# Performance work log

Hardware: AMD Instinct MI355X
Metric: run time of the kernel (lower is better)

Reference implementation:

```python
import jax, jax.numpy as jnp
import numpy as np

DIM = 512; HEADS = 8; DH = 64; M = 256; ITERS = 6; LN_EPS = 1e-5; RES_K = 33


def layernorm(x, g, b):
    mu = jnp.mean(x, -1, keepdims=True)
    var = jnp.mean((x - mu) ** 2, -1, keepdims=True)
    return (x - mu) * jax.lax.rsqrt(var + LN_EPS) * g + b


def moore_penrose_pinv(a, iters=ITERS):
    # Newton-Schulz iteration, matching nystrom_attention.moore_penrose_iter_pinv
    ab = jnp.abs(a)
    z = jnp.swapaxes(a, -1, -2) / (jnp.max(jnp.sum(ab, -1)) * jnp.max(jnp.sum(ab, -2)))
    I = jnp.eye(a.shape[-1], dtype=a.dtype)
    for _ in range(iters):
        az = a @ z
        z = 0.25 * z @ (13. * I - az @ (15. * I - az @ (7. * I - az)))
    return z


def dwconv2d(x, w, b, k):
    # x: [B,C,H,W], w: [C,1,k,k] depthwise
    C = x.shape[1]
    y = jax.lax.conv_general_dilated(x, w, (1, 1), [(k // 2, k // 2), (k // 2, k // 2)],
                                     feature_group_count=C,
                                     dimension_numbers=('NCHW', 'OIHW', 'NCHW'))
    return y + b[None, :, None, None]


def nystrom_attention(x, qkv_w, out_w, out_b, res_w):
    b, n, d = x.shape
    pad = (M - n % M) % M
    xp = jnp.pad(x, ((0, 0), (pad, 0), (0, 0)))  # pad at front, as in reference impl
    npd = n + pad
    qkv = xp @ qkv_w  # [b, npd, 3d]
    q, k, v = jnp.split(qkv, 3, axis=-1)
    to_heads = lambda t: t.reshape(b, npd, HEADS, DH).transpose(0, 2, 1, 3)  # bhnd
    q = to_heads(q) * (DH ** -0.5)
    k = to_heads(k)
    v = to_heads(v)
    l = npd // M  # tokens per landmark
    q_l = q.reshape(b, HEADS, M, l, DH).mean(3)  # [b,h,M,dh]
    k_l = k.reshape(b, HEADS, M, l, DH).mean(3)
    a1 = jax.nn.softmax(jnp.einsum('bhid,bhjd->bhij', q, k_l), axis=-1)    # [b,h,n,M]
    a2 = jax.nn.softmax(jnp.einsum('bhid,bhjd->bhij', q_l, k_l), axis=-1)  # [b,h,M,M]
    a3 = jax.nn.softmax(jnp.einsum('bhid,bhjd->bhij', q_l, k), axis=-1)    # [b,h,M,n]
    out = (a1 @ moore_penrose_pinv(a2)) @ (a3 @ v)  # [b,h,n,dh]
    # residual depthwise conv over sequence dim of v (channels = heads)
    res = jax.lax.conv_general_dilated(v, res_w, (1, 1), [(RES_K // 2, RES_K // 2), (0, 0)],
                                       feature_group_count=HEADS,
                                       dimension_numbers=('NCHW', 'OIHW', 'NCHW'))
    out = out + res
    out = out.transpose(0, 2, 1, 3).reshape(b, npd, d) @ out_w + out_b
    return out[:, -n:]


def _forward(x, fc1_w, fc1_b, cls_token,
             l1_norm_g, l1_norm_b, l1_qkv_w, l1_out_w, l1_out_b, l1_res_w,
             ppeg_w7, ppeg_b7, ppeg_w5, ppeg_b5, ppeg_w3, ppeg_b3,
             l2_norm_g, l2_norm_b, l2_qkv_w, l2_out_w, l2_out_b, l2_res_w,
             norm_g, norm_b, fc2_w, fc2_b):
    h = jax.nn.relu(x @ fc1_w + fc1_b)  # [B,N,C]
    B, N, C = h.shape
    Hs = int(np.ceil(np.sqrt(N)))
    add = Hs * Hs - N
    h = jnp.concatenate([h, h[:, :add]], axis=1)  # square padding
    cls = jnp.broadcast_to(cls_token, (B, 1, C))
    h = jnp.concatenate([cls, h], axis=1)  # [B, Hs*Hs+1, C]
    # TransLayer 1
    h = h + nystrom_attention(layernorm(h, l1_norm_g, l1_norm_b), l1_qkv_w, l1_out_w, l1_out_b, l1_res_w)
    # PPEG
    cls_t, feat = h[:, 0], h[:, 1:]
    cf = feat.transpose(0, 2, 1).reshape(B, C, Hs, Hs)
    y = cf + dwconv2d(cf, ppeg_w7, ppeg_b7, 7) + dwconv2d(cf, ppeg_w5, ppeg_b5, 5) + dwconv2d(cf, ppeg_w3, ppeg_b3, 3)
    h = jnp.concatenate([cls_t[:, None], y.reshape(B, C, Hs * Hs).transpose(0, 2, 1)], axis=1)
    # TransLayer 2
    h = h + nystrom_attention(layernorm(h, l2_norm_g, l2_norm_b), l2_qkv_w, l2_out_w, l2_out_b, l2_res_w)
    h = layernorm(h, norm_g, norm_b)[:, 0]
    return h @ fc2_w + fc2_b  # logits [B, n_classes]


def setup_inputs() -> dict:
    key = jax.random.key(0)
    ks = jax.random.split(key, 32)
    B, N, IN, C, NC = 1, 16384, 1024, 512, 4
    s = 0.02
    f32 = jnp.float32
    d = {}
    d['x'] = jax.random.normal(ks[0], (B, N, IN), f32)
    d['fc1_w'] = jax.random.normal(ks[1], (IN, C), f32) * s
    d['fc1_b'] = jnp.zeros((C,), f32)
    d['cls_token'] = jax.random.normal(ks[2], (1, 1, C), f32)
    for i, p in enumerate(['l1', 'l2']):
        kk = jax.random.split(ks[3 + i], 8)
        d[p + '_norm_g'] = jnp.ones((C,), f32)
        d[p + '_norm_b'] = jnp.zeros((C,), f32)
        d[p + '_qkv_w'] = jax.random.normal(kk[0], (C, 3 * C), f32) * s
        d[p + '_out_w'] = jax.random.normal(kk[1], (C, C), f32) * s
        d[p + '_out_b'] = jnp.zeros((C,), f32)
        d[p + '_res_w'] = jax.random.normal(kk[2], (HEADS, 1, RES_K, 1), f32) * s
    for i, k_sz in enumerate([7, 5, 3]):
        d[f'ppeg_w{k_sz}'] = jax.random.normal(ks[8 + i], (C, 1, k_sz, k_sz), f32) * s
        d[f'ppeg_b{k_sz}'] = jnp.zeros((C,), f32)
    d['norm_g'] = jnp.ones((C,), f32)
    d['norm_b'] = jnp.zeros((C,), f32)
    d['fc2_w'] = jax.random.normal(ks[12], (C, NC), f32) * s
    d['fc2_b'] = jnp.zeros((NC,), f32)
    return d


def reference(x, fc1_w, fc1_b, cls_token,
              l1_norm_g, l1_norm_b, l1_qkv_w, l1_out_w, l1_out_b, l1_res_w,
              ppeg_w7, ppeg_b7, ppeg_w5, ppeg_b5, ppeg_w3, ppeg_b3,
              l2_norm_g, l2_norm_b, l2_qkv_w, l2_out_w, l2_out_b, l2_res_w,
              norm_g, norm_b, fc2_w, fc2_b):
    return _forward(x, fc1_w, fc1_b, cls_token,
                    l1_norm_g, l1_norm_b, l1_qkv_w, l1_out_w, l1_out_b, l1_res_w,
                    ppeg_w7, ppeg_b7, ppeg_w5, ppeg_b5, ppeg_w3, ppeg_b3,
                    l2_norm_g, l2_norm_b, l2_qkv_w, l2_out_w, l2_out_b, l2_res_w,
                    norm_g, norm_b, fc2_w, fc2_b)
```

## Files before the change

### kernel.cpp

```cpp
#include <hip/hip_runtime.h>


#define NT 16385
#define NP 16640
#define PAD 255
#define CDIM 512
#define HEADS 8
#define DH 64
#define LM 256
#define LSEG 65

typedef unsigned short u16;
typedef unsigned int u32;
typedef __attribute__((ext_vector_type(8))) short bf16x8;
typedef __attribute__((ext_vector_type(4))) float f32x4;

__device__ __forceinline__ u16 f2b(float f){
  u32 u = __float_as_uint(f);
  u32 r = (u + 0x7FFFu + ((u >> 16) & 1u)) >> 16;
  return (u16)r;
}
__device__ __forceinline__ float b2f(u16 h){ return __uint_as_float(((u32)h) << 16); }

__device__ __forceinline__ void gload16(const u16* g, u16* l){
  __builtin_amdgcn_global_load_lds(
      (const __attribute__((address_space(1))) u32*)g,
      (__attribute__((address_space(3))) u32*)l, 16, 0, 0);
}

__device__ __forceinline__ int xcd_swz(int orig, int nwg){
  int qn = nwg >> 3, rn = nwg & 7;
  int xcd = orig & 7, sid = orig >> 3;
  return (xcd < rn ? xcd * (qn + 1) : rn * (qn + 1) + (xcd - rn) * qn) + sid;
}

__device__ __forceinline__ float wredSum(float v){
#pragma unroll
  for (int o = 32; o > 0; o >>= 1) v += __shfl_xor(v, o, 64);
  return v;
}
__device__ __forceinline__ float wredMax(float v){
#pragma unroll
  for (int o = 32; o > 0; o >>= 1) v = fmaxf(v, __shfl_xor(v, o, 64));
  return v;
}
__device__ __forceinline__ float bredSum(float v, float* sm){
  v = wredSum(v);
  int w = threadIdx.x >> 6, l = threadIdx.x & 63;
  __syncthreads();
  if (l == 0) sm[w] = v;
  __syncthreads();
  return sm[0] + sm[1] + sm[2] + sm[3];
}
__device__ __forceinline__ float bredMax(float v, float* sm){
  v = wredMax(v);
  int w = threadIdx.x >> 6, l = threadIdx.x & 63;
  __syncthreads();
  if (l == 0) sm[w] = v;
  __syncthreads();
  return fmaxf(fmaxf(sm[0], sm[1]), fmaxf(sm[2], sm[3]));
}

__global__ __launch_bounds__(256) void copy_cls_k(const float* __restrict__ cls,
                                                  float* __restrict__ h){
  h[threadIdx.x] = cls[threadIdx.x];
  h[threadIdx.x + 256] = cls[threadIdx.x + 256];
}
__global__ __launch_bounds__(256) void cvtbf_k(const float* __restrict__ in,
                                               u16* __restrict__ out, long long n){
  long long i = ((long long)blockIdx.x * 256 + threadIdx.x) * 4;
  long long stride = (long long)gridDim.x * 256 * 4;
  for (; i < n; i += stride){
    float4 v = *(const float4*)(in + i);
    out[i]     = f2b(v.x);
    out[i + 1] = f2b(v.y);
    out[i + 2] = f2b(v.z);
    out[i + 3] = f2b(v.w);
  }
}
__global__ __launch_bounds__(256) void tcbf_k(const float* __restrict__ in,
    u16* __restrict__ out, int R, int C, int ldin, int ldout,
    long long sIn, long long sOut){
  __shared__ float t[32][33];
  in += (long long)blockIdx.z * sIn; out += (long long)blockIdx.z * sOut;
  int c0 = blockIdx.x * 32, r0 = blockIdx.y * 32;
  int x = threadIdx.x & 31, y = threadIdx.x >> 5;
  for (int yy = y; yy < 32; yy += 8){
    int r = r0 + yy, c = c0 + x;
    if (r < R && c < C) t[yy][x] = in[(long long)r * ldin + c];
  }
  __syncthreads();
  for (int yy = y; yy < 32; yy += 8){
    int c = c0 + yy, r = r0 + x;
    if (c < C && r < R) out[(long long)c * ldout + r] = f2b(t[x][yy]);
  }
}

#define GB_STOREBF 1
#define GB_RELU    2
#define GB_ACCUM   4
#define GB_ATOMIC  8
#define GB_QSCALE  16
#define GB_SWZ     32

template<int DBUF>
__global__ __launch_bounds__(256) void gemmbf_k(
    const u16* __restrict__ A, const u16* __restrict__ B, void* __restrict__ Cv,
    int M, int N, int K, int lda, int ldb, int ldc,
    long long sA, long long sB, long long sC,
    const float* __restrict__ bias, const float* __restrict__ rowdiv, int sRow,
    float alpha, int flags, int ksplit, u16* __restrict__ vt)
{
  __shared__ __align__(16) u16 sh[DBUF ? 32768 : 16384];
  int zb = blockIdx.z / ksplit;
  int ks = blockIdx.z - zb * ksplit;
  A += (long long)zb * sA; B += (long long)zb * sB;
  float* Cf = (float*)Cv + (long long)zb * sC;
  u16*   Ch = (u16*)Cv + (long long)zb * sC;
  int klen = K / ksplit;
  int kbeg = ks * klen, kend = kbeg + klen;
  int tid = threadIdx.x;
  int w = tid >> 6, l = tid & 63;
  int row0, col0;
  if (flags & GB_SWZ){
    int gx = gridDim.x;
    int swz = xcd_swz(blockIdx.y * gx + blockIdx.x, gx * gridDim.y);
    row0 = (swz / gx) * 128; col0 = (swz % gx) * 128;
  } else {
    row0 = blockIdx.y * 128; col0 = blockIdx.x * 128;
  }
  int r8 = l >> 3;
  int csrc = ((l & 7) ^ r8) * 8;
  f32x4 acc[2][8];
#pragma unroll
  for (int i = 0; i < 2; i++)
#pragma unroll
    for (int j = 0; j < 8; j++) acc[i][j] = (f32x4){0.f, 0.f, 0.f, 0.f};

  int mrow = l & 15, q8 = l >> 4;

  auto STAGE = [&](int buf, int k0){
    u16* Asb = sh + buf * 16384;
    u16* Bsb = Asb + 8192;
#pragma unroll
    for (int c = 0; c < 4; c++){
      int r = w * 32 + c * 8;
      int gm = row0 + r + r8; if (gm >= M) gm = M - 1;
      gload16(A + (long long)gm * lda + k0 + csrc, &Asb[r * 64]);
      int gn = col0 + r + r8; if (gn >= N) gn = N - 1;
      gload16(B + (long long)gn * ldb + k0 + csrc, &Bsb[r * 64]);
    }
  };
  auto COMPUTE = [&](int buf){
    const u16* Asb = sh + buf * 16384;
    const u16* Bsb = Asb + 8192;
#pragma unroll
    for (int ks2 = 0; ks2 < 2; ks2++){
      int kc = ks2 * 4 + q8;
      bf16x8 af[2], bfr[8];
#pragma unroll
      for (int i = 0; i < 2; i++){
        int r = w * 32 + i * 16 + mrow;
        af[i] = *(const bf16x8*)&Asb[r * 64 + ((kc ^ (r & 7)) * 8)];
      }
#pragma unroll
      for (int j = 0; j < 8; j++){
        int r = j * 16 + mrow;
        bfr[j] = *(const bf16x8*)&Bsb[r * 64 + ((kc ^ (r & 7)) * 8)];
      }
#pragma unroll
      for (int i = 0; i < 2; i++)
#pragma unroll
        for (int j = 0; j < 8; j++)
          acc[i][j] = __builtin_amdgcn_mfma_f32_16x16x32_bf16(af[i], bfr[j], acc[i][j], 0, 0, 0);
    }
  };

  if constexpr (DBUF){
    STAGE(0, kbeg);
    __syncthreads();
    int cur = 0;
    for (int k0 = kbeg; k0 < kend; k0 += 64){
      if (k0 + 64 < kend) STAGE(cur ^ 1, k0 + 64);
      COMPUTE(cur);
      __syncthreads();
      cur ^= 1;
    }
  } else {
    for (int k0 = kbeg; k0 < kend; k0 += 64){
      STAGE(0, k0);
      __syncthreads();
      COMPUTE(0);
      __syncthreads();
    }
  }

  if (flags & GB_STOREBF){
#pragma unroll
    for (int p = 0; p < 2; p++){
      __syncthreads();
#pragma unroll
      for (int i = 0; i < 2; i++)
#pragma unroll
        for (int r = 0; r < 4; r++){
          int lrow = w * 32 + i * 16 + q8 * 4 + r;
          int gm = row0 + lrow;
          float rd = rowdiv ? rowdiv[(long long)zb * sRow + gm] : 1.f;
#pragma unroll
          for (int jj = 0; jj < 4; jj++){
            int j = p * 4 + jj;
            int gn = col0 + j * 16 + mrow;
            float v = alpha * acc[i][j][r];
            if ((flags & GB_QSCALE) && gn < 512) v *= 0.125f;
            if (rowdiv) v /= rd;
            if (bias) v += bias[gn];
            if (flags & GB_RELU) v = fmaxf(v, 0.f);
            sh[lrow * 72 + (j * 16 + mrow - p * 64)] = f2b(v);
          }
        }
      __syncthreads();
#pragma unroll
      for (int it = 0; it < 4; it++){
        int cidx = tid + it * 256;
        int rr = cidx >> 3, c8 = (cidx & 7) * 8;
        int gm = row0 + rr;
        if (gm < M)
          *(uint4*)(Ch + (long long)gm * ldc + col0 + p * 64 + c8) =
              *(const uint4*)&sh[rr * 72 + c8];
      }
    }
    if (vt && col0 >= 1024){
      int gc0 = col0 - 1024;
#pragma unroll
      for (int p = 0; p < 2; p++){
        __syncthreads();
#pragma unroll
        for (int i = 0; i < 2; i++)
#pragma unroll
          for (int r = 0; r < 4; r++){
            int lrow = w * 32 + i * 16 + q8 * 4 + r;
#pragma unroll
            for (int jj = 0; jj < 4; jj++){
              int j = p * 4 + jj;
              int lcol = j * 16 + mrow - p * 64;
              sh[lcol * 136 + lrow] = f2b(alpha * acc[i][j][r]);
            }
          }
        __syncthreads();
#pragma unroll
        for (int it = 0; it < 4; it++){
          int cidx = tid + it * 256;
          int cc = cidx >> 4, rc = (cidx & 15) * 8;
          *(uint4*)(vt + (long long)(gc0 + p * 64 + cc) * NP + row0 + rc) =
              *(const uint4*)&sh[cc * 136 + rc];
        }
      }
    }
    return;
  }

  if constexpr (DBUF){
    if (!(flags & GB_ATOMIC)){
      float* shf = (float*)sh;
#pragma unroll
      for (int p = 0; p < 2; p++){
        __syncthreads();
#pragma unroll
        for (int i = 0; i < 2; i++)
#pragma unroll
          for (int r = 0; r < 4; r++){
            int lrow = w * 32 + i * 16 + q8 * 4 + r;
            int gm = row0 + lrow;
            int gmc = (gm < M) ? gm : M - 1;
            float rd = rowdiv ? rowdiv[(long long)zb * sRow + gmc] : 1.f;
#pragma unroll
            for (int jj = 0; jj < 4; jj++){
              int j = p * 4 + jj;
              int gn = col0 + j * 16 + mrow;
              float v = alpha * acc[i][j][r];
              if ((flags & GB_QSCALE) && gn < 512) v *= 0.125f;
              if (rowdiv) v /= rd;
              if (bias) v += bias[gn];
              if (flags & GB_RELU) v = fmaxf(v, 0.f);
              shf[lrow * 68 + (j * 16 + mrow - p * 64)] = v;
            }
          }
        __syncthreads();
#pragma unroll
        for (int it = 0; it < 8; it++){
          int cidx = tid + it * 256;
          int rr = cidx >> 4, c4 = (cidx & 15) * 4;
          int gm = row0 + rr;
          if (gm >= M) continue;
          int gn = col0 + p * 64 + c4;
          if (gn + 3 < N){
            float4* dst = (float4*)(Cf + (long long)gm * ldc + gn);
            float4 vv = *(const float4*)&shf[rr * 68 + c4];
            if (flags & GB_ACCUM){
              float4 o = *dst;
              vv.x += o.x; vv.y += o.y; vv.z += o.z; vv.w += o.w;
            }
            *dst = vv;
          } else {
            for (int e = 0; e < 4; e++){
              if (gn + e >= N) break;
              float v = shf[rr * 68 + c4 + e];
              if (flags & GB_ACCUM) Cf[(long long)gm * ldc + gn + e] += v;
              else Cf[(long long)gm * ldc + gn + e] = v;
            }
          }
        }
      }
      return;
    }
  }

#pragma unroll
  for (int i = 0; i < 2; i++){
#pragma unroll
    for (int r = 0; r < 4; r++){
      int gm = row0 + w * 32 + i * 16 + q8 * 4 + r;
      if (gm >= M) continue;
      float rd = rowdiv ? rowdiv[(long long)zb * sRow + gm] : 1.f;
#pragma unroll
      for (int j = 0; j < 8; j++){
        int gn = col0 + j * 16 + mrow;
        if (gn >= N) continue;
        float v = alpha * acc[i][j][r];
        if ((flags & GB_QSCALE) && gn < 512) v *= 0.125f;
        if (rowdiv) v /= rd;
        if (bias) v += bias[gn];
        if (flags & GB_RELU) v = fmaxf(v, 0.f);
        long long ci = (long long)gm * ldc + gn;
        if (flags & GB_ATOMIC) atomicAdd(&Cf[ci], v);
        else if (flags & GB_ACCUM) Cf[ci] += v;
        else Cf[ci] = v;
      }
    }
  }
}

__device__ __forceinline__ void pinv_core(
    u16* lds, int cb, int rb, int head,
    const u16* __restrict__ Ah, const u16* __restrict__ Al,
    const u16* __restrict__ BTh, const u16* __restrict__ BTl,
    u16* __restrict__ Chh, u16* __restrict__ Cll,
    u16* __restrict__ CTh, u16* __restrict__ CTl,
    float* __restrict__ Cf,
    const u16* __restrict__ Avh, const u16* __restrict__ Avl,
    float dterm, float sterm, float eterm)
{
  u16* Ash = lds;
  u16* Asl = lds + 4096;
  u16* Bsh = lds + 8192;
  u16* Bsl = lds + 16384;
  long long off = (long long)head << 16;
  int tid = threadIdx.x, w = tid >> 6, l = tid & 63;
  int row0 = rb * 64, col0 = cb * 128;
  int r8 = l >> 3;
  int csrc = ((l & 7) ^ r8) * 8;
  int mrow = l & 15, q8 = l >> 4;
  f32x4 acc[8];
#pragma unroll
  for (int j = 0; j < 8; j++) acc[j] = (f32x4){0.f, 0.f, 0.f, 0.f};

  for (int k0 = 0; k0 < 256; k0 += 64){
#pragma unroll
    for (int c = 0; c < 2; c++){
      int r = w * 16 + c * 8;
      long long ga = off + (long long)(row0 + r + r8) * 256 + k0 + csrc;
      gload16(Ah + ga, &Ash[r * 64]);
      gload16(Al + ga, &Asl[r * 64]);
    }
#pragma unroll
    for (int c = 0; c < 4; c++){
      int r = w * 32 + c * 8;
      long long gb = off + (long long)(col0 + r + r8) * 256 + k0 + csrc;
      gload16(BTh + gb, &Bsh[r * 64]);
      gload16(BTl + gb, &Bsl[r * 64]);
    }
    __syncthreads();
#pragma unroll
    for (int ks2 = 0; ks2 < 2; ks2++){
      int kc = ks2 * 4 + q8;
      bf16x8 ah, al, bh[8], bl[8];
      {
        int r = w * 16 + mrow;
        int idx = r * 64 + ((kc ^ (r & 7)) * 8);
        ah = *(const bf16x8*)&Ash[idx];
        al = *(const bf16x8*)&Asl[idx];
      }
#pragma unroll
      for (int j = 0; j < 8; j++){
        int r = j * 16 + mrow;
        int idx = r * 64 + ((kc ^ (r & 7)) * 8);
        bh[j] = *(const bf16x8*)&Bsh[idx];
        bl[j] = *(const bf16x8*)&Bsl[idx];
      }
#pragma unroll
      for (int j = 0; j < 8; j++){
        acc[j] = __builtin_amdgcn_mfma_f32_16x16x32_bf16(ah, bh[j], acc[j], 0, 0, 0);
        acc[j] = __builtin_amdgcn_mfma_f32_16x16x32_bf16(ah, bl[j], acc[j], 0, 0, 0);
        acc[j] = __builtin_amdgcn_mfma_f32_16x16x32_bf16(al, bh[j], acc[j], 0, 0, 0);
      }
    }
    __syncthreads();
  }
#pragma unroll
  for (int r = 0; r < 4; r++){
    int gm = row0 + w * 16 + q8 * 4 + r;
#pragma unroll
    for (int j = 0; j < 8; j++){
      int gn = col0 + j * 16 + mrow;
      float v = sterm * acc[j][r];
      if (Avh){
        long long ai = off + (long long)gm * 256 + gn;
        v += eterm * (b2f(Avh[ai]) + b2f(Avl[ai]));
      }
      if (gm == gn) v += dterm;
      acc[j][r] = v;
      long long ci = off + (long long)gm * 256 + gn;
      if (Cf) Cf[ci] = v;
      if (Chh){
        u16 hi = f2b(v);
        Chh[ci] = hi;
        Cll[ci] = f2b(v - b2f(hi));
      }
    }
  }
  if (CTh){
#pragma unroll
    for (int pass = 0; pass < 2; pass++){
      __syncthreads();
#pragma unroll
      for (int r = 0; r < 4; r++){
        int lm = w * 16 + q8 * 4 + r;
#pragma unroll
        for (int j = 0; j < 8; j++){
          int ln = j * 16 + mrow;
          float v = acc[j][r];
          u16 hi = f2b(v);
          lds[ln * 72 + lm] = (pass == 0) ? hi : f2b(v - b2f(hi));
        }
      }
      __syncthreads();
      u16* dst = (pass == 0) ? CTh : CTl;
#pragma unroll
      for (int it = 0; it < 4; it++){
        int cidx = tid + it * 256;
        int rr = cidx >> 3;
        int cc = (cidx & 7) * 8;
        *(uint4*)(dst + off + (long long)(col0 + rr) * 256 + row0 + cc) =
            *(const uint4*)&lds[rr * 72 + cc];
      }
    }
  }
}

__global__ __launch_bounds__(256) void pinvh_k(
    const u16* __restrict__ Ah, const u16* __restrict__ Al,
    const u16* __restrict__ BTh, const u16* __restrict__ BTl,
    u16* __restrict__ Chh, u16* __restrict__ Cll,
    u16* __restrict__ CTh, u16* __restrict__ CTl,
    float* __restrict__ Cf,
    const u16* __restrict__ Avh, const u16* __restrict__ Avl,
    float dterm, float sterm, float eterm)
{
  __shared__ __align__(16) u16 lds[24576];
  pinv_core(lds, blockIdx.x, blockIdx.y, blockIdx.z,
            Ah, Al, BTh, BTl, Chh, Cll, CTh, CTl, Cf, Avh, Avl,
            dterm, sterm, eterm);
}
__global__ __launch_bounds__(256) void pinv2_k(
    const u16* __restrict__ azh, const u16* __restrict__ azl,
    const u16* __restrict__ azTh, const u16* __restrict__ azTl,
    const u16* __restrict__ zh, const u16* __restrict__ zl,
    u16* __restrict__ tATh, u16* __restrict__ tATl,
    u16* __restrict__ zah, u16* __restrict__ zal)
{
  __shared__ __align__(16) u16 lds[24576];
  int head = blockIdx.z & 7;
  if (blockIdx.z < 8)
    pinv_core(lds, blockIdx.x, blockIdx.y, head, azh, azl, azTh, azTl,
              nullptr, nullptr, tATh, tATl, nullptr, azh, azl, 15.f, 1.f, -7.f);
  else
    pinv_core(lds, blockIdx.x, blockIdx.y, head, zh, zl, azTh, azTl,
              zah, zal, nullptr, nullptr, nullptr, nullptr, nullptr, 0.f, 1.f, 0.f);
}

#define GF_TRANSB 1
__global__ __launch_bounds__(256) void gemm_k(
    const float* __restrict__ A, const float* __restrict__ B, float* __restrict__ C,
    int M, int N, int K, int lda, int ldb, int ldc,
    long long sA, long long sB, long long sC, float alpha, int flags)
{
  __shared__ __align__(16) float As[16][68];
  __shared__ __align__(16) float Bs[16][68];
  int zb = blockIdx.z;
  A += (long long)zb * sA; B += (long long)zb * sB; C += (long long)zb * sC;
  int tid = threadIdx.x;
  int tx = tid & 15, ty = tid >> 4;
  int row0 = blockIdx.y * 64, col0 = blockIdx.x * 64;
  float acc[4][4] = {};
  for (int k0 = 0; k0 < K; k0 += 16){
#pragma unroll
    for (int i = 0; i < 4; i++){
      int idx = tid + i * 256;
      int mm = idx >> 4, kk = idx & 15;
      int gm = row0 + mm;
      As[kk][mm] = (gm < M) ? A[(long long)gm * lda + (k0 + kk)] : 0.f;
    }
    if (!(flags & GF_TRANSB)){
#pragma unroll
      for (int i = 0; i < 4; i++){
        int idx = tid + i * 256;
        int kk = idx >> 6, nn = idx & 63;
        int gn = col0 + nn;
        Bs[kk][nn] = (gn < N) ? B[(long long)(k0 + kk) * ldb + gn] : 0.f;
      }
    } else {
#pragma unroll
      for (int i = 0; i < 4; i++){
        int idx = tid + i * 256;
        int nn = idx >> 4, kk = idx & 15;
        int gn = col0 + nn;
        Bs[kk][nn] = (gn < N) ? B[(long long)gn * ldb + (k0 + kk)] : 0.f;
      }
    }
    __syncthreads();
#pragma unroll
    for (int kk = 0; kk < 16; kk++){
      float4 av = *(const float4*)&As[kk][ty * 4];
      float4 bv = *(const float4*)&Bs[kk][tx * 4];
      float a[4] = {av.x, av.y, av.z, av.w};
      float b[4] = {bv.x, bv.y, bv.z, bv.w};
#pragma unroll
      for (int i = 0; i < 4; i++)
#pragma unroll
        for (int j = 0; j < 4; j++)
          acc[i][j] = fmaf(a[i], b[j], acc[i][j]);
    }
    __syncthreads();
  }
#pragma unroll
  for (int i = 0; i < 4; i++){
    int gm = row0 + ty * 4 + i;
    if (gm >= M) continue;
#pragma unroll
    for (int j = 0; j < 4; j++){
      int gn = col0 + tx * 4 + j;
      if (gn >= N) continue;
      C[(long long)gm * ldc + gn] = alpha * acc[i][j];
    }
  }
}

__global__ __launch_bounds__(256) void fattn_k(
    const u16* __restrict__ Qp, int ldq,
    const u16* __restrict__ Kp, int ldk,
    const u16* __restrict__ Vp, int ldv,
    long long sQh, long long sKh, long long sVh,
    int keysPerChunk,
    u16* __restrict__ outB, int ldo,
    float* __restrict__ O3, float* __restrict__ ML3, int nchunks, int qrows,
    int mode)
{
  __shared__ u16 Qs[64][72];
  __shared__ u16 Ks[128][72];
  __shared__ u16 Vs[64][136];
  __shared__ u16 Ps[4][16][136];
  int tid = threadIdx.x;
  int w = tid >> 6, l = tid & 63;
  int mrow = l & 15, q8 = l >> 4;
  int gx = gridDim.x, gy = gridDim.y;
  int swz = xcd_swz((blockIdx.z * gy + blockIdx.y) * gx + blockIdx.x,
                    gx * gy * gridDim.z);
  int qt = swz % gx, t2 = swz / gx;
  int ch = t2 % gy, h = t2 / gy;
  const u16* Q = Qp + (long long)h * sQh;
  const u16* K = Kp + (long long)h * sKh;
  const u16* V = Vp + (long long)h * sVh;
  int q0 = qt * 64;
  for (int i = tid; i < 512; i += 256){
    int r = i >> 3, c = (i & 7) * 8;
    *(uint4*)&Qs[r][c] = *(const uint4*)(Q + (long long)(q0 + r) * ldq + c);
  }
  float m_st[4], l_st[4];
  f32x4 acc_o[4];
#pragma unroll
  for (int r = 0; r < 4; r++){
    m_st[r] = -3.0e38f; l_st[r] = 0.f;
    acc_o[r] = (f32x4){0.f, 0.f, 0.f, 0.f};
  }
  int kbase = ch * keysPerChunk;
  for (int kt = 0; kt < keysPerChunk; kt += 128){
    for (int i = tid; i < 1024; i += 256){
      int r = i >> 3, c = (i & 7) * 8;
      *(uint4*)&Ks[r][c] = *(const uint4*)(K + (long long)(kbase + kt + r) * ldk + c);
    }
    for (int i = tid; i < 1024; i += 256){
      int r = i >> 4, c = (i & 15) * 8;
      *(uint4*)&Vs[r][c] = *(const uint4*)(V + (long long)r * ldv + kbase + kt + c);
    }
    __syncthreads();
    f32x4 accs[8];
#pragma unroll
    for (int j = 0; j < 8; j++) accs[j] = (f32x4){0.f, 0.f, 0.f, 0.f};
#pragma unroll
    for (int ks2 = 0; ks2 < 2; ks2++){
      bf16x8 af = *(const bf16x8*)&Qs[w * 16 + mrow][ks2 * 32 + q8 * 8];
#pragma unroll
      for (int j = 0; j < 8; j++){
        bf16x8 bfv = *(const bf16x8*)&Ks[j * 16 + mrow][ks2 * 32 + q8 * 8];
        accs[j] = __builtin_amdgcn_mfma_f32_16x16x32_bf16(af, bfv, accs[j], 0, 0, 0);
      }
    }
#pragma unroll
    for (int r = 0; r < 4; r++){
      float tm = -3.0e38f;
#pragma unroll
      for (int j = 0; j < 8; j++) tm = fmaxf(tm, accs[j][r]);
      tm = fmaxf(tm, __shfl_xor(tm, 1, 64));
      tm = fmaxf(tm, __shfl_xor(tm, 2, 64));
      tm = fmaxf(tm, __shfl_xor(tm, 4, 64));
      tm = fmaxf(tm, __shfl_xor(tm, 8, 64));
      float mn = fmaxf(m_st[r], tm);
      float al = __expf(m_st[r] - mn);
      m_st[r] = mn;
      float rs = 0.f;
#pragma unroll
      for (int j = 0; j < 8; j++){
        float e = __expf(accs[j][r] - mn);
        accs[j][r] = e;
        rs += e;
      }
      rs += __shfl_xor(rs, 1, 64);
      rs += __shfl_xor(rs, 2, 64);
      rs += __shfl_xor(rs, 4, 64);
      rs += __shfl_xor(rs, 8, 64);
      l_st[r] = al * l_st[r] + rs;
#pragma unroll
      for (int j = 0; j < 4; j++) acc_o[j][r] *= al;
    }
#pragma unroll
    for (int j = 0; j < 8; j++)
#pragma unroll
      for (int r = 0; r < 4; r++)
        Ps[w][q8 * 4 + r][j * 16 + mrow] = f2b(accs[j][r]);
    __syncthreads();
#pragma unroll
    for (int kc = 0; kc < 4; kc++){
      bf16x8 af = *(const bf16x8*)&Ps[w][mrow][kc * 32 + q8 * 8];
#pragma unroll
      for (int j = 0; j < 4; j++){
        bf16x8 bfv = *(const bf16x8*)&Vs[j * 16 + mrow][kc * 32 + q8 * 8];
        acc_o[j] = __builtin_amdgcn_mfma_f32_16x16x32_bf16(af, bfv, acc_o[j], 0, 0, 0);
      }
    }
    __syncthreads();
  }
  if (mode == 0){
#pragma unroll
    for (int r = 0; r < 4; r++){
      int grow = q0 + w * 16 + q8 * 4 + r;
      float inv = 1.f / l_st[r];
#pragma unroll
      for (int j = 0; j < 4; j++)
        outB[(long long)grow * ldo + h * 64 + j * 16 + mrow] = f2b(acc_o[j][r] * inv);
    }
  } else {
#pragma unroll
    for (int r = 0; r < 4; r++){
      int row = q0 + w * 16 + q8 * 4 + r;
      long long b = ((long long)h * nchunks + ch) * qrows + row;
#pragma unroll
      for (int j = 0; j < 4; j++)
        O3[b * 64 + j * 16 + mrow] = acc_o[j][r];
      if (mrow == 0){
        ML3[b * 2] = m_st[r];
        ML3[b * 2 + 1] = l_st[r];
      }
    }
  }
}

__global__ __launch_bounds__(256) void comb3_k(
    const float* __restrict__ O3, const float* __restrict__ ML3,
    float* __restrict__ a3v)
{
  int h = blockIdx.y;
  int row = blockIdx.x * 4 + (threadIdx.x >> 6);
  int d = threadIdx.x & 63;
  float m = -3.0e38f;
  for (int c = 0; c < 13; c++)
    m = fmaxf(m, ML3[(((long long)h * 13 + c) * 256 + row) * 2]);
  float l = 0.f, o = 0.f;
  for (int c = 0; c < 13; c++){
    long long b = ((long long)h * 13 + c) * 256 + row;
    float wgt = __expf(ML3[b * 2] - m);
    l += wgt * ML3[b * 2 + 1];
    o += wgt * O3[b * 64 + d];
  }
  a3v[((long long)h * 256 + row) * 64 + d] = o / l;
}

__global__ __launch_bounds__(256) void ln_pad_k(
    const float* __restrict__ h, const float* __restrict__ g,
    const float* __restrict__ b, u16* __restrict__ out)
{
  __shared__ float sm[4];
  int row = blockIdx.x, tid = threadIdx.x;
  u16* o = out + (long long)row * CDIM;
  if (row < PAD){ o[tid] = 0; o[tid + 256] = 0; return; }
  const float* x = h + (long long)(row - PAD) * CDIM;
  float v0 = x[tid], v1 = x[tid + 256];
  float s = bredSum(v0 + v1, sm);
  float s2 = bredSum(v0 * v0 + v1 * v1, sm);
  float mean = s * (1.f / 512.f);
  float var = s2 * (1.f / 512.f) - mean * mean;
  float rstd = rsqrtf(var + 1e-5f);
  o[tid] = f2b((v0 - mean) * rstd * g[tid] + b[tid]);
  o[tid + 256] = f2b((v1 - mean) * rstd * g[tid + 256] + b[tid + 256]);
}

__global__ __launch_bounds__(256) void landmark_k(
    const u16* __restrict__ qkv, float* __restrict__ ql, float* __restrict__ kl,
    u16* __restrict__ qlh, u16* __restrict__ klh)
{
  int m = blockIdx.x * 2 + (threadIdx.x >> 7);
  int c8 = (threadIdx.x & 127) * 8;
  const u16* base = qkv + (long long)(m * LSEG) * 1536 + c8;
  float s[8] = {};
  for (int j = 0; j < LSEG; j++){
    uint4 pk = *(const uint4*)(base + (long long)j * 1536);
    const u16* pv = (const u16*)&pk;
#pragma unroll
    for (int e = 0; e < 8; e++) s[e] += b2f(pv[e]);
  }
#pragma unroll
  for (int e = 0; e < 8; e++){
    int col = c8 + e;
    float v = s[e] * (1.f / 65.f);
    int h = (col & 511) >> 6, d = col & 63;
    int idx = (h * LM + m) * DH + d;
    if (col < 512){ ql[idx] = v; qlh[idx] = f2b(v); }
    else          { kl[idx] = v; klh[idx] = f2b(v); }
  }
}

__global__ __launch_bounds__(256) void softmax256_k(float* __restrict__ S,
    u16* __restrict__ a2h, u16* __restrict__ a2l, float* __restrict__ scal)
{
  __shared__ float sm[4];
  int i = blockIdx.x, h = blockIdx.y, j = threadIdx.x;
  if (i == 0 && h == 0 && j < 2) scal[j] = 0.f;
  long long idx = ((long long)h * LM + i) * 256 + j;
  float v = S[idx];
  float m = bredMax(v, sm);
  float e = __expf(v - m);
  float s = bredSum(e, sm);
  float p = e / s;
  S[idx] = p;
  u16 hi = f2b(p);
  a2h[idx] = hi;
  a2l[idx] = f2b(p - b2f(hi));
}

__global__ __launch_bounds__(256) void pinv_scal_k(
    const float* __restrict__ a2, float* __restrict__ scal)
{
  __shared__ float sm[4];
  int h = blockIdx.x, i = threadIdx.x;
  const float* Ah = a2 + (long long)h * 65536;
  float rs = 0.f, cs = 0.f;
  for (int j = 0; j < 256; j++){
    rs += fabsf(Ah[i * 256 + j]);
    cs += fabsf(Ah[j * 256 + i]);
  }
  float rmax = bredMax(rs, sm);
  __syncthreads();
  float cmax = bredMax(cs, sm);
  if (i == 0){
    atomicMax((int*)&scal[0], __float_as_int(rmax));
    atomicMax((int*)&scal[1], __float_as_int(cmax));
  }
}

__global__ __launch_bounds__(256) void z0_k(
    const float* __restrict__ a2, const float* __restrict__ scal,
    u16* __restrict__ zh, u16* __restrict__ zl,
    u16* __restrict__ zTh, u16* __restrict__ zTl)
{
  int ri = blockIdx.x, h = blockIdx.y, j = threadIdx.x;
  float inv = 1.f / (scal[0] * scal[1]);
  long long base = ((long long)h * LM + ri) * 256;
  float v = a2[base + j] * inv;
  u16 hi = f2b(v), lo = f2b(v - b2f(hi));
  zTh[base + j] = hi; zTl[base + j] = lo;
  long long tb = ((long long)h * LM + j) * 256 + ri;
  zh[tb] = hi; zl[tb] = lo;
}

__global__ __launch_bounds__(256) void resconv_k(
    const u16* __restrict__ vT, const float* __restrict__ rw,
    u16* __restrict__ attn)
{
  int c = blockIdx.x * 256 + threadIdx.x;
  int s0 = blockIdx.y * 8;
  int h = c >> 6;
  float w[33];
#pragma unroll
  for (int t = 0; t < 33; t++) w[t] = rw[h * 33 + t];
  float vr[40];
  const u16* vrow = vT + (long long)c * NP;
  if (s0 >= 16 && s0 + 24 <= NP){
#pragma unroll
    for (int q = 0; q < 5; q++){
      uint4 pk = *(const uint4*)(vrow + s0 - 16 + q * 8);
      const u16* pv = (const u16*)&pk;
#pragma unroll
      for (int e = 0; e < 8; e++) vr[q * 8 + e] = b2f(pv[e]);
    }
  } else {
#pragma unroll
    for (int j = 0; j < 40; j++){
      int s = s0 - 16 + j;
      vr[j] = (s >= 0 && s < NP) ? b2f(vrow[s]) : 0.f;
    }
  }
#pragma unroll
  for (int i = 0; i < 8; i++){
    float a = 0.f;
#pragma unroll
    for (int t = 0; t < 33; t++) a = fmaf(vr[i + t], w[t], a);
    long long idx = (long long)(s0 + i) * CDIM + c;
    attn[idx] = f2b(b2f(attn[idx]) + a);
  }
}

__global__ __launch_bounds__(256) void transpose_k(
    const float* __restrict__ in, float* __restrict__ out, int R, int Cc)
{
  __shared__ float t[32][33];
  int bx = blockIdx.x * 32, by = blockIdx.y * 32;
  int x = threadIdx.x & 31, y4 = threadIdx.x >> 5;
  for (int yy = y4; yy < 32; yy += 8){
    int r = by + yy, c = bx + x;
    if (r < R && c < Cc) t[yy][x] = in[(long long)r * Cc + c];
  }
  __syncthreads();
  for (int yy = y4; yy < 32; yy += 8){
    int r = bx + yy, c = by + x;
    if (r < Cc && c < R) out[(long long)r * R + c] = t[x][yy];
  }
}

__global__ __launch_bounds__(256) void ppeg_k(
    const float* __restrict__ cf, float* __restrict__ yt,
    const float* __restrict__ w7, const float* __restrict__ b7,
    const float* __restrict__ w5, const float* __restrict__ b5,
    const float* __restrict__ w3, const float* __restrict__ b3)
{
  __shared__ float tile[22][23];
  int c = blockIdx.z;
  int ty0 = blockIdx.y * 16, tx0 = blockIdx.x * 16;
  const float* img = cf + (long long)c * 16384;
  for (int i = threadIdx.x; i < 22 * 22; i += 256){
    int yy = i / 22, xx = i - yy * 22;
    int gy = ty0 - 3 + yy, gx = tx0 - 3 + xx;
    tile[yy][xx] = (gy >= 0 && gy < 128 && gx >= 0 && gx < 128) ? img[gy * 128 + gx] : 0.f;
  }
  __syncthreads();
  int lx = threadIdx.x & 15, ly = threadIdx.x >> 4;
  float o = tile[ly + 3][lx + 3] + b7[c] + b5[c] + b3[c];
  const float* W7 = w7 + c * 49;
#pragma unroll
  for (int ky = 0; ky < 7; ky++)
#pragma unroll
    for (int kx = 0; kx < 7; kx++)
      o = fmaf(tile[ly + ky][lx + kx], W7[ky * 7 + kx], o);
  const float* W5 = w5 + c * 25;
#pragma unroll
  for (int ky = 0; ky < 5; ky++)
#pragma unroll
    for (int kx = 0; kx < 5; kx++)
      o = fmaf(tile[ly + 1 + ky][lx + 1 + kx], W5[ky * 5 + kx], o);
  const float* W3 = w3 + c * 9;
#pragma unroll
  for (int ky = 0; ky < 3; ky++)
#pragma unroll
    for (int kx = 0; kx < 3; kx++)
      o = fmaf(tile[ly + 2 + ky][lx + 2 + kx], W3[ky * 3 + kx], o);
  yt[(long long)c * 16384 + (ty0 + ly) * 128 + (tx0 + lx)] = o;
}

__global__ __launch_bounds__(256) void final_k(
    const float* __restrict__ h, const float* __restrict__ g,
    const float* __restrict__ b, const float* __restrict__ w,
    const float* __restrict__ bias, float* __restrict__ out)
{
  __shared__ float sm[4];
  __shared__ float pj[256][4];
  int tid = threadIdx.x;
  float v0 = h[tid], v1 = h[tid + 256];
  float s = bredSum(v0 + v1, sm);
  float s2 = bredSum(v0 * v0 + v1 * v1, sm);
  float mean = s * (1.f / 512.f);
  float var = s2 * (1.f / 512.f) - mean * mean;
  float rstd = rsqrtf(var + 1e-5f);
  float n0 = (v0 - mean) * rstd * g[tid] + b[tid];
  float n1 = (v1 - mean) * rstd * g[tid + 256] + b[tid + 256];
#pragma unroll
  for (int j = 0; j < 4; j++)
    pj[tid][j] = n0 * w[tid * 4 + j] + n1 * w[(tid + 256) * 4 + j];
  __syncthreads();
  if (tid < 4){
    float acc = 0.f;
    for (int k = 0; k < 256; k++) acc += pj[k][tid];
    out[tid] = acc + bias[tid];
  }
}

static inline void gemmbf(hipStream_t st, const u16* A, const u16* B, void* C,
                          int M, int N, int K, int lda, int ldb, int ldc,
                          long long sA, long long sB, long long sC, int batch,
                          const float* bias, const float* rowdiv, int sRow,
                          float alpha, int flags, int ksplit, u16* vt, int dbuf)
{
  dim3 grid((N + 127) / 128, (M + 127) / 128, batch * ksplit);
  if (dbuf)
    gemmbf_k<1><<<grid, 256, 0, st>>>(A, B, C, M, N, K, lda, ldb, ldc, sA, sB, sC,
                                      bias, rowdiv, sRow, alpha, flags, ksplit, vt);
  else
    gemmbf_k<0><<<grid, 256, 0, st>>>(A, B, C, M, N, K, lda, ldb, ldc, sA, sB, sC,
                                      bias, rowdiv, sRow, alpha, flags, ksplit, vt);
}

#define B_H     0LL
#define B_XQ    33556480LL
#define B_ATTN  50595840LL
#define B_QKV   67635200LL
#define B_VT    118753280LL
#define B_O3    135792640LL
#define B_ML3   142608384LL
#define B_QL    169871360LL
#define B_KL    170395648LL
#define B_QLH   170919936LL
#define B_KLH   171182080LL
#define B_A2    171444224LL
#define B_PV2   173541376LL
#define B_A3V   184027136LL
#define B_Z2    184551424LL
#define B_Z2T   185075712LL
#define B_SCAL  185604096LL
#define B_W1T   185604352LL
#define B_WQT   186652928LL
#define B_WOT   188225792LL
#define WS_REQ  188750080LL
#define MB1     1048576LL

extern "C" void kernel_launch(void* const* d_in, const int* in_sizes, int n_in,
                              void* d_out, int out_size, void* d_ws, size_t ws_size,
                              hipStream_t stream)
{
  (void)in_sizes; (void)n_in; (void)out_size;
  if (ws_size < (size_t)WS_REQ) return;

  const float* x      = (const float*)d_in[0];
  const float* fc1_w  = (const float*)d_in[1];
  const float* fc1_b  = (const float*)d_in[2];
  const float* cls    = (const float*)d_in[3];
  const float* l_ng[2]  = {(const float*)d_in[4],  (const float*)d_in[10]};
  const float* l_nb[2]  = {(const float*)d_in[5],  (const float*)d_in[11]};
  const float* l_qkv[2] = {(const float*)d_in[6],  (const float*)d_in[12]};
  const float* l_ow[2]  = {(const float*)d_in[7],  (const float*)d_in[13]};
  const float* l_ob[2]  = {(const float*)d_in[8],  (const float*)d_in[14]};
  const float* l_rw[2]  = {(const float*)d_in[9],  (const float*)d_in[15]};
  const float* w7 = (const float*)d_in[16];
  const float* b7 = (const float*)d_in[17];
  const float* w5 = (const float*)d_in[18];
  const float* b5 = (const float*)d_in[19];
  const float* w3 = (const float*)d_in[20];
  const float* b3 = (const float*)d_in[21];
  const float* norm_g = (const float*)d_in[22];
  const float* norm_b = (const float*)d_in[23];
  const float* fc2_w  = (const float*)d_in[24];
  const float* fc2_b  = (const float*)d_in[25];
  float* out = (float*)d_out;

  char* WB = (char*)d_ws;
  float* h    = (float*)(WB + B_H);
  u16*   xq   = (u16*)(WB + B_XQ);
  u16*   attnb= (u16*)(WB + B_ATTN);
  u16*   qkvb = (u16*)(WB + B_QKV);
  u16*   xb   = (u16*)(WB + B_QKV);
  float* cf   = (float*)(WB + B_QKV);
  float* yt   = (float*)(WB + B_QKV + 33554432LL);
  u16*   vT   = (u16*)(WB + B_VT);
  float* O3   = (float*)(WB + B_O3);
  float* ML3  = (float*)(WB + B_ML3);
  float* ql   = (float*)(WB + B_QL);
  float* kl   = (float*)(WB + B_KL);
  u16*   qlh  = (u16*)(WB + B_QLH);
  u16*   klh  = (u16*)(WB + B_KLH);
  float* a2   = (float*)(WB + B_A2);
  float* a3v  = (float*)(WB + B_A3V);
  float* Z2   = (float*)(WB + B_Z2);
  u16*   Z2T  = (u16*)(WB + B_Z2T);
  float* scal = (float*)(WB + B_SCAL);
  u16*   w1T  = (u16*)(WB + B_W1T);
  u16*   wqT  = (u16*)(WB + B_WQT);
  u16*   woT  = (u16*)(WB + B_WOT);

  u16* a2h  = (u16*)(WB + B_XQ + 0 * MB1);
  u16* a2l  = (u16*)(WB + B_XQ + 1 * MB1);
  u16* z0h  = (u16*)(WB + B_XQ + 2 * MB1);
  u16* z0l  = (u16*)(WB + B_XQ + 3 * MB1);
  u16* z0Th = (u16*)(WB + B_XQ + 4 * MB1);
  u16* z0Tl = (u16*)(WB + B_XQ + 5 * MB1);
  u16* z1h  = (u16*)(WB + B_XQ + 6 * MB1);
  u16* z1l  = (u16*)(WB + B_XQ + 7 * MB1);
  u16* z1Th = (u16*)(WB + B_XQ + 8 * MB1);
  u16* z1Tl = (u16*)(WB + B_XQ + 9 * MB1);
  u16* azh  = (u16*)(WB + B_XQ + 10 * MB1);
  u16* azl  = (u16*)(WB + B_XQ + 11 * MB1);
  u16* azTh = (u16*)(WB + B_XQ + 12 * MB1);
  u16* azTl = (u16*)(WB + B_XQ + 13 * MB1);
  u16* tATh = (u16*)(WB + B_XQ + 14 * MB1);
  u16* tATl = (u16*)(WB + B_XQ + 15 * MB1);
  u16* zah  = (u16*)(WB + B_PV2 + 0 * MB1);
  u16* zal  = (u16*)(WB + B_PV2 + 1 * MB1);
  float* zf = (float*)(WB + B_PV2 + 2 * MB1);

  copy_cls_k<<<1, 256, 0, stream>>>(cls, h);
  cvtbf_k<<<4096, 256, 0, stream>>>(x, xb, 16384LL * 1024);
  tcbf_k<<<dim3(16, 32, 1), 256, 0, stream>>>(fc1_w, w1T, 1024, 512, 512, 1024, 0, 0);
  gemmbf(stream, xb, w1T, h + CDIM, 16384, 512, 1024, 1024, 1024, 512,
         0, 0, 0, 1, fc1_b, nullptr, 0, 1.f, GB_RELU, 1, nullptr, 1);

  for (int L = 0; L < 2; L++){
    ln_pad_k<<<NP, 256, 0, stream>>>(h, l_ng[L], l_nb[L], xq);
    tcbf_k<<<dim3(48, 16, 1), 256, 0, stream>>>(l_qkv[L], wqT, 512, 1536, 1536, 512, 0, 0);
    gemmbf(stream, xq, wqT, qkvb, NP, 1536, 512, 512, 512, 1536,
           0, 0, 0, 1, nullptr, nullptr, 0, 1.f, GB_STOREBF | GB_QSCALE | GB_SWZ, 1, vT, 1);
    landmark_k<<<LM / 2, 256, 0, stream>>>(qkvb, ql, kl, qlh, klh);
    gemm_k<<<dim3(4, 4, 8), 256, 0, stream>>>(ql, kl, a2, LM, LM, DH, DH, DH, LM,
                                              16384, 16384, 65536, 1.f, GF_TRANSB);
    softmax256_k<<<dim3(LM, HEADS), 256, 0, stream>>>(a2, a2h, a2l, scal);
    pinv_scal_k<<<HEADS, 256, 0, stream>>>(a2, scal);
    z0_k<<<dim3(LM, HEADS), 256, 0, stream>>>(a2, scal, z0h, z0l, z0Th, z0Tl);
    u16 *zh = z0h, *zl = z0l, *zTh = z0Th, *zTl = z0Tl;
    u16 *nzh = z1h, *nzl = z1l, *nzTh = z1Th, *nzTl = z1Tl;
    dim3 pg(2, 4, HEADS), pg2(2, 4, 2 * HEADS);
    for (int it = 0; it < 6; it++){
      pinvh_k<<<pg, 256, 0, stream>>>(a2h, a2l, zTh, zTl,
                                      azh, azl, azTh, azTl, nullptr,
                                      nullptr, nullptr, 0.f, 1.f, 0.f);
      pinv2_k<<<pg2, 256, 0, stream>>>(azh, azl, azTh, azTl, zh, zl,
                                       tATh, tATl, zah, zal);
      pinvh_k<<<pg, 256, 0, stream>>>(zah, zal, tATh, tATl,
                                      nzh, nzl, nzTh, nzTl,
                                      (it == 5) ? zf : nullptr,
                                      zh, zl, 0.f, -0.25f, 3.25f);
      u16* t;
      t = zh; zh = nzh; nzh = t;   t = zl; zl = nzl; nzl = t;
      t = zTh; zTh = nzTh; nzTh = t; t = zTl; zTl = nzTl; nzTl = t;
    }
    fattn_k<<<dim3(4, 13, 8), 256, 0, stream>>>(
        qlh, 64, qkvb + 512, 1536, vT, NP,
        16384, 64, 64LL * NP, 1280,
        nullptr, 0, O3, ML3, 13, 256, 1);
    comb3_k<<<dim3(64, 8), 256, 0, stream>>>(O3, ML3, a3v);
    gemm_k<<<dim3(1, 4, 8), 256, 0, stream>>>(zf, a3v, Z2, LM, DH, LM, LM, DH, DH,
                                              65536, 16384, 16384, 1.f, 0);
    tcbf_k<<<dim3(2, 8, 8), 256, 0, stream>>>(Z2, Z2T, 256, 64, 64, 256, 16384, 16384);
    fattn_k<<<dim3(260, 1, 8), 256, 0, stream>>>(
        qkvb, 1536, klh, 64, Z2T, 256,
        64, 16384, 16384, 256,
        attnb, CDIM, nullptr, nullptr, 1, NP, 0);
    resconv_k<<<dim3(2, NP / 8), 256, 0, stream>>>(vT, l_rw[L], attnb);
    tcbf_k<<<dim3(16, 16, 1), 256, 0, stream>>>(l_ow[L], woT, 512, 512, 512, 512, 0, 0);
    gemmbf(stream, attnb + (long long)PAD * CDIM, woT, h, NT, CDIM, CDIM,
           CDIM, CDIM, CDIM, 0, 0, 0, 1, l_ob[L], nullptr, 0, 1.f, GB_ACCUM, 1, nullptr, 1);

    if (L == 0){
      transpose_k<<<dim3(16, 512), 256, 0, stream>>>(h + CDIM, cf, 16384, CDIM);
      ppeg_k<<<dim3(8, 8, CDIM), 256, 0, stream>>>(cf, yt, w7, b7, w5, b5, w3, b3);
      transpose_k<<<dim3(512, 16), 256, 0, stream>>>(yt, h + CDIM, CDIM, 16384);
    }
  }

  final_k<<<1, 256, 0, stream>>>(h, norm_g, norm_b, fc2_w, fc2_b, out);
}
```

Before: 1.463 ms.

## Shrink pinv tiles with double-buffered LDS and register-block PPEG conv

The pinv GEMM core now uses 64x64 output tiles instead of 64x128, which doubles the grid so more workgroups cover the small 256x256 per-head matrices. It also double-buffers the K-loop staging in LDS, so the next tile loads while the current one computes. Separately, the PPEG depthwise conv kernel now processes full 128-wide rows in 16-row strips, caches the weights in LDS, and has each thread accumulate 8 vertical outputs from a shared column of registers. Together these aim to cut pinv latency from low occupancy and serialized loads, and to cut redundant LDS reads in the conv, at the cost of more LDS per block.

```diff
diff --git a/kernel.cpp b/kernel.cpp
--- a/kernel.cpp
+++ b/kernel.cpp
@@ -350,40 +350,41 @@
     const u16* __restrict__ Avh, const u16* __restrict__ Avl,
     float dterm, float sterm, float eterm)
 {
-  u16* Ash = lds;
-  u16* Asl = lds + 4096;
-  u16* Bsh = lds + 8192;
-  u16* Bsl = lds + 16384;
   long long off = (long long)head << 16;
   int tid = threadIdx.x, w = tid >> 6, l = tid & 63;
-  int row0 = rb * 64, col0 = cb * 128;
+  int row0 = rb * 64, col0 = cb * 64;
   int r8 = l >> 3;
   int csrc = ((l & 7) ^ r8) * 8;
   int mrow = l & 15, q8 = l >> 4;
-  f32x4 acc[8];
-#pragma unroll
-  for (int j = 0; j < 8; j++) acc[j] = (f32x4){0.f, 0.f, 0.f, 0.f};
-
-  for (int k0 = 0; k0 < 256; k0 += 64){
+  f32x4 acc[4];
+#pragma unroll
+  for (int j = 0; j < 4; j++) acc[j] = (f32x4){0.f, 0.f, 0.f, 0.f};
+
+  auto STAGE = [&](int buf, int k0){
+    u16* Ash = lds + buf * 16384;
+    u16* Asl = Ash + 4096;
+    u16* Bsh = Ash + 8192;
+    u16* Bsl = Ash + 12288;
 #pragma unroll
     for (int c = 0; c < 2; c++){
       int r = w * 16 + c * 8;
       long long ga = off + (long long)(row0 + r + r8) * 256 + k0 + csrc;
       gload16(Ah + ga, &Ash[r * 64]);
       gload16(Al + ga, &Asl[r * 64]);
-    }
-#pragma unroll
-    for (int c = 0; c < 4; c++){
-      int r = w * 32 + c * 8;
       long long gb = off + (long long)(col0 + r + r8) * 256 + k0 + csrc;
       gload16(BTh + gb, &Bsh[r * 64]);
       gload16(BTl + gb, &Bsl[r * 64]);
     }
-    __syncthreads();
+  };
+  auto COMPUTE = [&](int buf){
+    const u16* Ash = lds + buf * 16384;
+    const u16* Asl = Ash + 4096;
+    const u16* Bsh = Ash + 8192;
+    const u16* Bsl = Ash + 12288;
 #pragma unroll
     for (int ks2 = 0; ks2 < 2; ks2++){
       int kc = ks2 * 4 + q8;
-      bf16x8 ah, al, bh[8], bl[8];
+      bf16x8 ah, al, bh[4], bl[4];
       {
         int r = w * 16 + mrow;
         int idx = r * 64 + ((kc ^ (r & 7)) * 8);
@@ -391,26 +392,36 @@
         al = *(const bf16x8*)&Asl[idx];
       }
 #pragma unroll
-      for (int j = 0; j < 8; j++){
+      for (int j = 0; j < 4; j++){
         int r = j * 16 + mrow;
         int idx = r * 64 + ((kc ^ (r & 7)) * 8);
         bh[j] = *(const bf16x8*)&Bsh[idx];
         bl[j] = *(const bf16x8*)&Bsl[idx];
       }
 #pragma unroll
-      for (int j = 0; j < 8; j++){
+      for (int j = 0; j < 4; j++){
         acc[j] = __builtin_amdgcn_mfma_f32_16x16x32_bf16(ah, bh[j], acc[j], 0, 0, 0);
         acc[j] = __builtin_amdgcn_mfma_f32_16x16x32_bf16(ah, bl[j], acc[j], 0, 0, 0);
         acc[j] = __builtin_amdgcn_mfma_f32_16x16x32_bf16(al, bh[j], acc[j], 0, 0, 0);
       }
     }
+  };
+
+  STAGE(0, 0);
+  __syncthreads();
+  int cur = 0;
+  for (int k0 = 0; k0 < 256; k0 += 64){
+    if (k0 + 64 < 256) STAGE(cur ^ 1, k0 + 64);
+    COMPUTE(cur);
     __syncthreads();
-  }
+    cur ^= 1;
+  }
+
 #pragma unroll
   for (int r = 0; r < 4; r++){
     int gm = row0 + w * 16 + q8 * 4 + r;
 #pragma unroll
-    for (int j = 0; j < 8; j++){
+    for (int j = 0; j < 4; j++){
       int gn = col0 + j * 16 + mrow;
       float v = sterm * acc[j][r];
       if (Avh){
@@ -436,7 +447,7 @@
       for (int r = 0; r < 4; r++){
         int lm = w * 16 + q8 * 4 + r;
 #pragma unroll
-        for (int j = 0; j < 8; j++){
+        for (int j = 0; j < 4; j++){
           int ln = j * 16 + mrow;
           float v = acc[j][r];
           u16 hi = f2b(v);
@@ -446,7 +457,7 @@
       __syncthreads();
       u16* dst = (pass == 0) ? CTh : CTl;
 #pragma unroll
-      for (int it = 0; it < 4; it++){
+      for (int it = 0; it < 2; it++){
         int cidx = tid + it * 256;
         int rr = cidx >> 3;
         int cc = (cidx & 7) * 8;
@@ -466,7 +477,7 @@
     const u16* __restrict__ Avh, const u16* __restrict__ Avl,
     float dterm, float sterm, float eterm)
 {
-  __shared__ __align__(16) u16 lds[24576];
+  __shared__ __align__(16) u16 lds[32768];
   pinv_core(lds, blockIdx.x, blockIdx.y, blockIdx.z,
             Ah, Al, BTh, BTl, Chh, Cll, CTh, CTl, Cf, Avh, Avl,
             dterm, sterm, eterm);
@@ -478,7 +489,7 @@
     u16* __restrict__ tATh, u16* __restrict__ tATl,
     u16* __restrict__ zah, u16* __restrict__ zal)
 {
-  __shared__ __align__(16) u16 lds[24576];
+  __shared__ __align__(16) u16 lds[32768];
   int head = blockIdx.z & 7;
   if (blockIdx.z < 8)
     pinv_core(lds, blockIdx.x, blockIdx.y, head, azh, azl, azTh, azTl,
@@ -861,37 +872,64 @@
     const float* __restrict__ w5, const float* __restrict__ b5,
     const float* __restrict__ w3, const float* __restrict__ b3)
 {
-  __shared__ float tile[22][23];
-  int c = blockIdx.z;
-  int ty0 = blockIdx.y * 16, tx0 = blockIdx.x * 16;
+  __shared__ float tile[22][136];
+  __shared__ float wsh[84];
+  int c = blockIdx.y;
+  int ys = blockIdx.x * 16;
+  int tid = threadIdx.x;
   const float* img = cf + (long long)c * 16384;
-  for (int i = threadIdx.x; i < 22 * 22; i += 256){
-    int yy = i / 22, xx = i - yy * 22;
-    int gy = ty0 - 3 + yy, gx = tx0 - 3 + xx;
+  if (tid < 49) wsh[tid] = w7[c * 49 + tid];
+  else if (tid >= 64 && tid < 89) wsh[49 + tid - 64] = w5[c * 25 + (tid - 64)];
+  else if (tid >= 96 && tid < 105) wsh[74 + tid - 96] = w3[c * 9 + (tid - 96)];
+  else if (tid == 128) wsh[83] = b7[c] + b5[c] + b3[c];
+  for (int i = tid; i < 22 * 134; i += 256){
+    int yy = i / 134, xx = i - yy * 134;
+    int gy = ys - 3 + yy, gx = xx - 3;
     tile[yy][xx] = (gy >= 0 && gy < 128 && gx >= 0 && gx < 128) ? img[gy * 128 + gx] : 0.f;
   }
   __syncthreads();
-  int lx = threadIdx.x & 15, ly = threadIdx.x >> 4;
-  float o = tile[ly + 3][lx + 3] + b7[c] + b5[c] + b3[c];
-  const float* W7 = w7 + c * 49;
-#pragma unroll
-  for (int ky = 0; ky < 7; ky++)
-#pragma unroll
-    for (int kx = 0; kx < 7; kx++)
-      o = fmaf(tile[ly + ky][lx + kx], W7[ky * 7 + kx], o);
-  const float* W5 = w5 + c * 25;
-#pragma unroll
-  for (int ky = 0; ky < 5; ky++)
-#pragma unroll
-    for (int kx = 0; kx < 5; kx++)
-      o = fmaf(tile[ly + 1 + ky][lx + 1 + kx], W5[ky * 5 + kx], o);
-  const float* W3 = w3 + c * 9;
-#pragma unroll
-  for (int ky = 0; ky < 3; ky++)
-#pragma unroll
-    for (int kx = 0; kx < 3; kx++)
-      o = fmaf(tile[ly + 2 + ky][lx + 2 + kx], W3[ky * 3 + kx], o);
-  yt[(long long)c * 16384 + (ty0 + ly) * 128 + (tx0 + lx)] = o;
+  int x = tid & 127;
+  int yo = (tid >> 7) * 8;
+  float acc[8];
+#pragma unroll
+  for (int i = 0; i < 8; i++) acc[i] = tile[yo + i + 3][x + 3] + wsh[83];
+#pragma unroll
+  for (int kx = 0; kx < 7; kx++){
+    float col[14];
+#pragma unroll
+    for (int t = 0; t < 14; t++) col[t] = tile[yo + t][x + kx];
+    float wc7[7];
+#pragma unroll
+    for (int ky = 0; ky < 7; ky++) wc7[ky] = wsh[ky * 7 + kx];
+#pragma unroll
+    for (int i = 0; i < 8; i++)
+#pragma unroll
+      for (int ky = 0; ky < 7; ky++)
+        acc[i] = fmaf(col[i + ky], wc7[ky], acc[i]);
+    if (kx >= 1 && kx <= 5){
+      float wc5[5];
+#pragma unroll
+      for (int ky = 0; ky < 5; ky++) wc5[ky] = wsh[49 + ky * 5 + (kx - 1)];
+#pragma unroll
+      for (int i = 0; i < 8; i++)
+#pragma unroll
+        for (int ky = 0; ky < 5; ky++)
+          acc[i] = fmaf(col[i + 1 + ky], wc5[ky], acc[i]);
+    }
+    if (kx >= 2 && kx <= 4){
+      float wc3[3];
+#pragma unroll
+      for (int ky = 0; ky < 3; ky++) wc3[ky] = wsh[74 + ky * 3 + (kx - 2)];
+#pragma unroll
+      for (int i = 0; i < 8; i++)
+#pragma unroll
+        for (int ky = 0; ky < 3; ky++)
+          acc[i] = fmaf(col[i + 2 + ky], wc3[ky], acc[i]);
+    }
+  }
+  float* dst = yt + (long long)c * 16384 + (ys + yo) * 128 + x;
+#pragma unroll
+  for (int i = 0; i < 8; i++) dst[i * 128] = acc[i];
 }
 
 __global__ __launch_bounds__(256) void final_k(
@@ -1051,7 +1089,7 @@
     z0_k<<<dim3(LM, HEADS), 256, 0, stream>>>(a2, scal, z0h, z0l, z0Th, z0Tl);
     u16 *zh = z0h, *zl = z0l, *zTh = z0Th, *zTl = z0Tl;
     u16 *nzh = z1h, *nzl = z1l, *nzTh = z1Th, *nzTl = z1Tl;
-    dim3 pg(2, 4, HEADS), pg2(2, 4, 2 * HEADS);
+    dim3 pg(4, 4, HEADS), pg2(4, 4, 2 * HEADS);
     for (int it = 0; it < 6; it++){
       pinvh_k<<<pg, 256, 0, stream>>>(a2h, a2l, zTh, zTl,
                                       azh, azl, azTh, azTl, nullptr,
@@ -1085,7 +1123,7 @@
 
     if (L == 0){
       transpose_k<<<dim3(16, 512), 256, 0, stream>>>(h + CDIM, cf, 16384, CDIM);
-      ppeg_k<<<dim3(8, 8, CDIM), 256, 0, stream>>>(cf, yt, w7, b7, w5, b5, w3, b3);
+      ppeg_k<<<dim3(8, 512), 256, 0, stream>>>(cf, yt, w7, b7, w5, b5, w3, b3);
       transpose_k<<<dim3(512, 16), 256, 0, stream>>>(yt, h + CDIM, CDIM, 16384);
     }
   }
```

New measurement: 1.252 ms. 1.17x faster.
